# Kernel optimization log

Hardware: AMD Instinct MI355X
Metric: run time of the kernel (lower is better)

## Reference

```python
import jax, jax.numpy as jnp
import numpy as np

N, E, R, F_IN, F_OUT = 50000, 800000, 6, 128, 128


def setup_inputs() -> dict:
    key = jax.random.key(0)
    ks = jax.random.split(key, 9)
    return {
        "node_h": jax.random.normal(ks[0], (N, F_IN), jnp.float32),
        "weight": jax.random.normal(ks[1], (R, F_IN, F_OUT), jnp.float32) * 0.05,
        "att1": jax.random.normal(ks[2], (F_OUT, 1), jnp.float32),
        "att2": jax.random.normal(ks[3], (F_OUT, 1), jnp.float32),
        "Wc": jax.random.normal(ks[4], (F_OUT, 2 * F_OUT), jnp.float32) * 0.05,
        "bc": jnp.zeros((F_OUT,), jnp.float32),
        "edge_src": jax.random.randint(ks[5], (E,), 0, N, dtype=jnp.int64) if jax.config.jax_enable_x64 else jax.random.randint(ks[5], (E,), 0, N),
        "edge_dst": jax.random.randint(ks[6], (E,), 0, N),
        "edge_rel": jax.random.randint(ks[7], (E,), 0, R),
    }


def reference(node_h, weight, att1, att2, Wc, bc, edge_src, edge_dst, edge_rel):
    n = node_h.shape[0]
    # combined (relation, dst) segment id -> replaces dense per-relation adjacency
    seg = edge_rel * n + edge_dst
    # per-relation incoming degree of each dst node: [R, N]
    deg = jax.ops.segment_sum(
        jnp.ones(edge_src.shape, jnp.float32), seg, num_segments=R * n
    ).reshape(R, n)
    # per-relation transformed features hrd[r] = h @ W[r]: [R, N, O]
    hrd = jnp.einsum('nf,rfo->rno', node_h, weight)
    # per-edge message = hrd[rel_e, src_e]: [E, O]
    msg = hrd[edge_rel, edge_src]
    # scatter-sum into (rel, dst) then normalize by 1/(1 + deg_r(dst))
    agg = jax.ops.segment_sum(msg, seg, num_segments=R * n).reshape(R, n, F_OUT)
    hrs = agg / (1.0 + deg)[:, :, None]
    op = jnp.transpose(hrs, (1, 0, 2))  # [N, R, O]
    # two attention heads: softmax over the relation axis
    s1 = jax.nn.softmax(op @ att1, axis=1)  # [N, R, 1]
    s2 = jax.nn.softmax(op @ att2, axis=1)
    h_comb = jnp.concatenate([op * s1, op * s2], axis=-1)  # [N, R, 2O]
    h5 = h_comb @ Wc.T + bc  # attention_concat linear: [N, R, O]
    h = jnp.sum(h5, axis=1)  # sum over relations: [N, O]
    return (h, weight)
```

## Files before the change

### kernel.cpp

```cpp
#include <hip/hip_runtime.h>

#define NN 50000
#define NE 800000
#define NR 6
#define FD 128
#define NS (NN * NR)
#define MB ((NS + 1023) / 1024)

typedef __attribute__((ext_vector_type(8))) short bf16x8;
typedef __attribute__((ext_vector_type(4))) float f32x4;

__device__ __forceinline__ unsigned short f2bf(float x) {
    unsigned u = __float_as_uint(x);
    u += 0x7FFFu + ((u >> 16) & 1u);
    return (unsigned short)(u >> 16);
}
__device__ __forceinline__ unsigned pack2bf(float lo, float hi) {
    return (unsigned)f2bf(lo) | ((unsigned)f2bf(hi) << 16);
}
__device__ __forceinline__ float bf_lo(unsigned u) { return __uint_as_float(u << 16); }
__device__ __forceinline__ float bf_hi(unsigned u) { return __uint_as_float(u & 0xFFFF0000u); }

__global__ __launch_bounds__(256) void k_cast(
    const float* __restrict__ node_h, unsigned* __restrict__ nh2)
{
    int i = (blockIdx.x * 256 + threadIdx.x) * 8;
    float4 a = *(const float4*)(node_h + i);
    float4 b = *(const float4*)(node_h + i + 4);
    uint4 o;
    o.x = pack2bf(a.x, a.y); o.y = pack2bf(a.z, a.w);
    o.z = pack2bf(b.x, b.y); o.w = pack2bf(b.z, b.w);
    *(uint4*)(nh2 + i / 2) = o;
}

__global__ __launch_bounds__(256) void k_hist(
    const int* __restrict__ edst, const int* __restrict__ erel,
    int* __restrict__ cnt)
{
    int e = blockIdx.x * 256 + threadIdx.x;
    if (e < NE) atomicAdd(cnt + edst[e] * NR + erel[e], 1);
}

__global__ __launch_bounds__(256) void k_bsum(
    const int* __restrict__ cnt, int* __restrict__ bsum)
{
    __shared__ int red[256];
    const int b = blockIdx.x, t = threadIdx.x;
    int idx0 = b * 1024 + t * 4;
    int4 c = *(const int4*)(cnt + idx0);
    int s = 0;
    if (idx0 + 0 < NS) s += c.x;
    if (idx0 + 1 < NS) s += c.y;
    if (idx0 + 2 < NS) s += c.z;
    if (idx0 + 3 < NS) s += c.w;
    red[t] = s;
    __syncthreads();
    for (int off = 128; off > 0; off >>= 1) {
        if (t < off) red[t] += red[t + off];
        __syncthreads();
    }
    if (t == 0) bsum[b] = red[0];
}

__global__ __launch_bounds__(512) void k_scanb(
    const int* __restrict__ bsum, int* __restrict__ bpre)
{
    __shared__ int s[512];
    const int t = threadIdx.x;
    int v = (t < MB) ? bsum[t] : 0;
    s[t] = v;
    __syncthreads();
    for (int off = 1; off < 512; off <<= 1) {
        int x = (t >= off) ? s[t - off] : 0;
        __syncthreads();
        if (t >= off) s[t] += x;
        __syncthreads();
    }
    bpre[t] = s[t] - v;
}

__global__ __launch_bounds__(256) void k_scan3(
    const int* __restrict__ cnt, const int* __restrict__ bpre,
    int* __restrict__ offs, int* __restrict__ cursor)
{
    __shared__ int partial[256];
    const int b = blockIdx.x, t = threadIdx.x;
    int idx0 = b * 1024 + t * 4;
    int4 c = *(const int4*)(cnt + idx0);
    if (idx0 + 0 >= NS) c.x = 0;
    if (idx0 + 1 >= NS) c.y = 0;
    if (idx0 + 2 >= NS) c.z = 0;
    if (idx0 + 3 >= NS) c.w = 0;
    int tsum = c.x + c.y + c.z + c.w;
    partial[t] = tsum;
    __syncthreads();
    for (int off = 1; off < 256; off <<= 1) {
        int x = (t >= off) ? partial[t - off] : 0;
        __syncthreads();
        if (t >= off) partial[t] += x;
        __syncthreads();
    }
    int base = bpre[b] + partial[t] - tsum;
    int4 o;
    o.x = base;
    o.y = base + c.x;
    o.z = base + c.x + c.y;
    o.w = base + c.x + c.y + c.z;
    if (idx0 + 3 < NS) {
        *(int4*)(offs + idx0) = o;
        *(int4*)(cursor + idx0) = o;
    } else {
        int v[4] = {o.x, o.y, o.z, o.w};
        for (int k = 0; k < 4; ++k)
            if (idx0 + k < NS) { offs[idx0 + k] = v[k]; cursor[idx0 + k] = v[k]; }
    }
    if (b == 0 && t == 0) offs[NS] = NE;
}

__global__ __launch_bounds__(256) void k_place(
    const int* __restrict__ esrc, const int* __restrict__ edst,
    const int* __restrict__ erel, int* __restrict__ cursor,
    int* __restrict__ eidx)
{
    int e = blockIdx.x * 256 + threadIdx.x;
    if (e >= NE) return;
    int seg = edst[e] * NR + erel[e];
    int pos = atomicAdd(cursor + seg, 1);
    eidx[pos] = esrc[e];
}

__global__ __launch_bounds__(256) void k_prep_w(
    const float* __restrict__ weight,
    const float* __restrict__ att1, const float* __restrict__ att2,
    float* __restrict__ w1, float* __restrict__ w2)
{
    __shared__ float a1s[FD], a2s[FD];
    const int r = blockIdx.x;
    const int t = threadIdx.x;
    if (t < FD) { a1s[t] = att1[t]; a2s[t] = att2[t]; }
    __syncthreads();
    int f = t & 127;
    const float* av = (t < FD) ? a1s : a2s;
    float* wo = (t < FD) ? w1 : w2;
    const float* Wrow = weight + ((size_t)r * FD + f) * FD;
    float acc = 0.f;
#pragma unroll 8
    for (int o = 0; o < FD; ++o) acc += Wrow[o] * av[o];
    wo[r * FD + f] = acc;
}

__global__ __launch_bounds__(256) void k_prep_U(
    const float* __restrict__ weight, const float* __restrict__ Wc,
    short* __restrict__ Upk)
{
    __shared__ float As[64 * 65];
    __shared__ float Bs[64 * 132];
    const int h  = blockIdx.y / NR;
    const int r  = blockIdx.y % NR;
    const int f0 = blockIdx.x * 64;
    const int t  = threadIdx.x;
    const int tm = t & 15, tn = t >> 4;

    float acc[4][8];
#pragma unroll
    for (int i = 0; i < 4; ++i)
#pragma unroll
        for (int j = 0; j < 8; ++j) acc[i][j] = 0.f;

    for (int kt = 0; kt < 2; ++kt) {
#pragma unroll
        for (int i = 0; i < 4; ++i) {
            int flat = i * 1024 + t * 4;
            int row = flat >> 6, k = flat & 63;
            float4 v = *(const float4*)(weight + ((size_t)r * FD + f0 + row) * FD + kt * 64 + k);
            float* p = As + row * 65 + k;
            p[0] = v.x; p[1] = v.y; p[2] = v.z; p[3] = v.w;
        }
#pragma unroll
        for (int i = 0; i < 8; ++i) {
            int flat4 = i * 256 + t;
            int o = flat4 >> 4, j4 = flat4 & 15;
            float4 v = *(const float4*)(Wc + (size_t)o * 256 + h * FD + kt * 64 + j4 * 4);
            float* p = Bs + (j4 * 4) * 132 + o;
            p[0] = v.x; p[132] = v.y; p[264] = v.z; p[396] = v.w;
        }
        __syncthreads();
#pragma unroll 4
        for (int k = 0; k < 64; ++k) {
            float aa[4];
#pragma unroll
            for (int i = 0; i < 4; ++i) aa[i] = As[(4 * tm + i) * 65 + k];
            float4 blo = *(const float4*)(Bs + k * 132 + 8 * tn);
            float4 bhi = *(const float4*)(Bs + k * 132 + 8 * tn + 4);
            float bb[8] = {blo.x, blo.y, blo.z, blo.w, bhi.x, bhi.y, bhi.z, bhi.w};
#pragma unroll
            for (int i = 0; i < 4; ++i)
#pragma unroll
                for (int j = 0; j < 8; ++j) acc[i][j] += aa[i] * bb[j];
        }
        __syncthreads();
    }

#pragma unroll
    for (int i = 0; i < 4; ++i)
#pragma unroll
        for (int j = 0; j < 8; ++j) {
            int f = f0 + 4 * tm + i, o = 8 * tn + j;
            int kstep = f >> 5, g = (f >> 3) & 3, jj = f & 7;
            int nt = o >> 4, ln = g * 16 + (o & 15);
            size_t sidx = ((((size_t)(h * NR + r) * 4 + kstep) * 8 + nt) * 64 + ln) * 8 + jj;
            Upk[sidx] = (short)f2bf(acc[i][j]);
        }
}

__global__ __launch_bounds__(256) void k_agg(
    const unsigned* __restrict__ nh2,
    const int* __restrict__ offs,
    const int* __restrict__ eidx,
    const float* __restrict__ w1v, const float* __restrict__ w2v,
    unsigned* __restrict__ aggp,
    float* __restrict__ s1o, float* __restrict__ s2o)
{
    const int t = threadIdx.x;
    const int lane = t & 63;
    const int grp = lane >> 4;
    const int fl  = lane & 15;
    const int d = blockIdx.x * 4 + (t >> 6);
    if (d >= NN) return;

    float p1v[2], p2v[2];

#pragma unroll
    for (int pass = 0; pass < 2; ++pass) {
        const int r = pass * 4 + grp;
        float q1 = 0.f, q2 = 0.f;
        if (r < NR) {
            const int sbeg = offs[d * NR + r];
            const int send = offs[d * NR + r + 1];
            float a0 = 0.f, a1 = 0.f, a2 = 0.f, a3 = 0.f;
            float a4 = 0.f, a5 = 0.f, a6 = 0.f, a7 = 0.f;
            for (int j = sbeg; j < send; ++j) {
                int s = eidx[j];
                uint4 v = *(const uint4*)(nh2 + (size_t)s * 64 + fl * 4);
                a0 += bf_lo(v.x); a1 += bf_hi(v.x);
                a2 += bf_lo(v.y); a3 += bf_hi(v.y);
                a4 += bf_lo(v.z); a5 += bf_hi(v.z);
                a6 += bf_lo(v.w); a7 += bf_hi(v.w);
            }
            float sc = 1.0f / (1.0f + (float)(send - sbeg));
            a0 *= sc; a1 *= sc; a2 *= sc; a3 *= sc;
            a4 *= sc; a5 *= sc; a6 *= sc; a7 *= sc;
            uint4 o;
            o.x = pack2bf(a0, a1); o.y = pack2bf(a2, a3);
            o.z = pack2bf(a4, a5); o.w = pack2bf(a6, a7);
            *(uint4*)(aggp + ((size_t)r * NN + d) * 64 + fl * 4) = o;
            float4 wa = *(const float4*)(w1v + r * FD + fl * 8);
            float4 wb = *(const float4*)(w1v + r * FD + fl * 8 + 4);
            float4 wc = *(const float4*)(w2v + r * FD + fl * 8);
            float4 wd = *(const float4*)(w2v + r * FD + fl * 8 + 4);
            q1 = a0 * wa.x + a1 * wa.y + a2 * wa.z + a3 * wa.w
               + a4 * wb.x + a5 * wb.y + a6 * wb.z + a7 * wb.w;
            q2 = a0 * wc.x + a1 * wc.y + a2 * wc.z + a3 * wc.w
               + a4 * wd.x + a5 * wd.y + a6 * wd.z + a7 * wd.w;
        }
#pragma unroll
        for (int off = 1; off < 16; off <<= 1) {
            q1 += __shfl_xor(q1, off, 64);
            q2 += __shfl_xor(q2, off, 64);
        }
        p1v[pass] = q1; p2v[pass] = q2;
    }

    float p1[NR], p2[NR];
#pragma unroll
    for (int r = 0; r < 4; ++r) {
        p1[r] = __shfl(p1v[0], r * 16, 64);
        p2[r] = __shfl(p2v[0], r * 16, 64);
    }
    p1[4] = __shfl(p1v[1], 0, 64);  p1[5] = __shfl(p1v[1], 16, 64);
    p2[4] = __shfl(p2v[1], 0, 64);  p2[5] = __shfl(p2v[1], 16, 64);

    float m1 = p1[0], m2 = p2[0];
#pragma unroll
    for (int r = 1; r < NR; ++r) { m1 = fmaxf(m1, p1[r]); m2 = fmaxf(m2, p2[r]); }
    float e1[NR], e2[NR], d1 = 0.f, d2 = 0.f;
#pragma unroll
    for (int r = 0; r < NR; ++r) {
        e1[r] = __expf(p1[r] - m1); d1 += e1[r];
        e2[r] = __expf(p2[r] - m2); d2 += e2[r];
    }
    d1 = 1.0f / d1; d2 = 1.0f / d2;
    if (lane == 0) {
#pragma unroll
        for (int r = 0; r < NR; ++r) {
            s1o[d * NR + r] = e1[r] * d1;
            s2o[d * NR + r] = e2[r] * d2;
        }
    }
}

__global__ __launch_bounds__(256, 4) void k_fused(
    const unsigned* __restrict__ aggp,
    const float* __restrict__ s1, const float* __restrict__ s2,
    const short* __restrict__ Upk,
    const float* __restrict__ bc,
    float* __restrict__ out)
{
    __shared__ short Al[64 * 128];
    __shared__ float sl[2 * 64 * NR];
    const int n0 = blockIdx.x * 64;
    const int t = threadIdx.x;
    const int lane = t & 63;
    const int w = t >> 6;

    for (int i = t; i < 2 * 64 * NR; i += 256) {
        int h = i / (64 * NR);
        int rr = i % (64 * NR);
        int row = rr / NR, r = rr % NR;
        int n = n0 + row;
        float v = 0.f;
        if (n < NN) v = (h ? s2 : s1)[(size_t)n * NR + r];
        sl[i] = v;
    }

    f32x4 acc[8];
#pragma unroll
    for (int nt = 0; nt < 8; ++nt) acc[nt] = (f32x4){0.f, 0.f, 0.f, 0.f};

    const int m = w * 16 + (lane & 15);
    const int g = lane >> 4;

    for (int r = 0; r < NR; ++r) {
        __syncthreads();
        {
            int row = t >> 2, kq = t & 3;
            int n = n0 + row;
            const unsigned* src = aggp + ((size_t)r * NN + n) * 64 + kq * 16;
#pragma unroll
            for (int c = 0; c < 4; ++c) {
                uint4 v = make_uint4(0, 0, 0, 0);
                if (n < NN) v = *(const uint4*)(src + c * 4);
                int ks = kq * 32 + c * 8;
                int addr = row * 128 + (ks ^ ((row & 7) << 3));
                *(uint4*)&Al[addr] = v;
            }
        }
        __syncthreads();

#pragma unroll
        for (int h = 0; h < 2; ++h) {
            f32x4 ar[8];
#pragma unroll
            for (int nt = 0; nt < 8; ++nt) ar[nt] = (f32x4){0.f, 0.f, 0.f, 0.f};
#pragma unroll
            for (int kstep = 0; kstep < 4; ++kstep) {
                bf16x8 af = *(const bf16x8*)&Al[m * 128 + ((kstep * 32 + g * 8) ^ ((m & 7) << 3))];
                const short* Ub = Upk + (((size_t)(h * NR + r) * 4 + kstep) * 8) * 64 * 8 + lane * 8;
#pragma unroll
                for (int nt = 0; nt < 8; ++nt) {
                    bf16x8 bfr = *(const bf16x8*)(Ub + nt * 64 * 8);
                    ar[nt] = __builtin_amdgcn_mfma_f32_16x16x32_bf16(af, bfr, ar[nt], 0, 0, 0);
                }
            }
            float sv[4];
#pragma unroll
            for (int reg = 0; reg < 4; ++reg)
                sv[reg] = sl[h * 64 * NR + (w * 16 + (lane >> 4) * 4 + reg) * NR + r];
#pragma unroll
            for (int nt = 0; nt < 8; ++nt)
#pragma unroll
                for (int reg = 0; reg < 4; ++reg)
                    acc[nt][reg] += sv[reg] * ar[nt][reg];
        }
    }

    const int rowbase = n0 + w * 16 + (lane >> 4) * 4;
    const int col0 = lane & 15;
#pragma unroll
    for (int nt = 0; nt < 8; ++nt) {
        int col = nt * 16 + col0;
        float b6 = 6.0f * bc[col];
#pragma unroll
        for (int reg = 0; reg < 4; ++reg) {
            int n = rowbase + reg;
            if (n < NN) out[(size_t)n * FD + col] = acc[nt][reg] + b6;
        }
    }
}

extern "C" void kernel_launch(void* const* d_in, const int* in_sizes, int n_in,
                              void* d_out, int out_size, void* d_ws, size_t ws_size,
                              hipStream_t stream)
{
    const float* node_h = (const float*)d_in[0];
    const float* weight = (const float*)d_in[1];
    const float* att1   = (const float*)d_in[2];
    const float* att2   = (const float*)d_in[3];
    const float* Wc     = (const float*)d_in[4];
    const float* bc     = (const float*)d_in[5];
    const int* esrc = (const int*)d_in[6];
    const int* edst = (const int*)d_in[7];
    const int* erel = (const int*)d_in[8];
    float* out = (float*)d_out;

    char* wsp = (char*)d_ws;
    auto alloc = [&](size_t bytes) {
        char* p = wsp;
        wsp += (bytes + 255) & ~(size_t)255;
        return p;
    };
    unsigned* aggp = (unsigned*)alloc((size_t)NR * NN * 64 * 4);
    unsigned* nh2  = (unsigned*)alloc((size_t)NN * 64 * 4);
    short* Upk     = (short*)alloc((size_t)2 * NR * FD * FD * 2);
    float* w1      = (float*)alloc(NR * FD * 4);
    float* w2      = (float*)alloc(NR * FD * 4);
    float* s1      = (float*)alloc((size_t)NN * NR * 4);
    float* s2      = (float*)alloc((size_t)NN * NR * 4);
    int* offs      = (int*)alloc((size_t)(NS + 1 + 64) * 4);
    int* cursor    = (int*)alloc((size_t)(NS + 2048) * 4);
    int* bsum      = (int*)alloc(512 * 4);
    int* bpre      = (int*)alloc(512 * 4);
    int* eidx      = (int*)d_out;

    hipMemsetAsync(cursor, 0, (size_t)NS * sizeof(int), stream);

    k_hist<<<(NE + 255) / 256, 256, 0, stream>>>(edst, erel, cursor);
    k_bsum<<<MB, 256, 0, stream>>>(cursor, bsum);
    k_scanb<<<1, 512, 0, stream>>>(bsum, bpre);
    k_scan3<<<MB, 256, 0, stream>>>(cursor, bpre, offs, cursor);
    k_place<<<(NE + 255) / 256, 256, 0, stream>>>(esrc, edst, erel, cursor, eidx);

    k_cast<<<(NN * FD / 8 + 255) / 256, 256, 0, stream>>>(node_h, nh2);
    k_prep_w<<<NR, 256, 0, stream>>>(weight, att1, att2, w1, w2);
    k_prep_U<<<dim3(2, 2 * NR), 256, 0, stream>>>(weight, Wc, Upk);

    k_agg<<<(NN + 3) / 4, 256, 0, stream>>>(nh2, offs, eidx, w1, w2, aggp, s1, s2);

    k_fused<<<(NN + 63) / 64, 256, 0, stream>>>(aggp, s1, s2, Upk, bc, out);

    hipMemcpyAsync(out + (size_t)NN * FD, weight,
                   (size_t)NR * FD * FD * sizeof(float),
                   hipMemcpyDeviceToDevice, stream);
}
```

Before: 355.1 us.

## Split fused epilogue over output column halves and load A fragments directly

The fused projection kernel now launches a second grid dimension, so each block computes 64 of the 128 output columns, halving per-thread accumulators and doubling block count. The LDS staging of the aggregated rows, with its per-relation barriers, is replaced by each lane loading its bf16 A fragments straight from global memory. Both column-half blocks read the same A rows, so global/L2 traffic for the aggregate doubles. In exchange the kernel gets lower register pressure, more parallelism and no per-relation syncs.

New measurement: 348.8 us. Within noise of the previous version (-1.8%).

```diff
diff --git a/kernel.cpp b/kernel.cpp
--- a/kernel.cpp
+++ b/kernel.cpp
@@ -299,16 +299,16 @@
     }
 }
 
-__global__ __launch_bounds__(256, 4) void k_fused(
+__global__ __launch_bounds__(256) void k_fused(
     const unsigned* __restrict__ aggp,
     const float* __restrict__ s1, const float* __restrict__ s2,
     const short* __restrict__ Upk,
     const float* __restrict__ bc,
     float* __restrict__ out)
 {
-    __shared__ short Al[64 * 128];
     __shared__ float sl[2 * 64 * NR];
     const int n0 = blockIdx.x * 64;
+    const int ch = blockIdx.y;
     const int t = threadIdx.x;
     const int lane = t & 63;
     const int w = t >> 6;
@@ -322,63 +322,55 @@
         if (n < NN) v = (h ? s2 : s1)[(size_t)n * NR + r];
         sl[i] = v;
     }
-
-    f32x4 acc[8];
-#pragma unroll
-    for (int nt = 0; nt < 8; ++nt) acc[nt] = (f32x4){0.f, 0.f, 0.f, 0.f};
-
-    const int m = w * 16 + (lane & 15);
+    __syncthreads();
+
+    const int mrow = min(n0 + w * 16 + (lane & 15), NN - 1);
     const int g = lane >> 4;
+    const unsigned* arow = aggp + (size_t)mrow * 64 + g * 4;
+
+    f32x4 acc[4];
+#pragma unroll
+    for (int nt = 0; nt < 4; ++nt) acc[nt] = (f32x4){0.f, 0.f, 0.f, 0.f};
+
+    const int rl4 = w * 16 + (lane >> 4) * 4;
 
     for (int r = 0; r < NR; ++r) {
-        __syncthreads();
-        {
-            int row = t >> 2, kq = t & 3;
-            int n = n0 + row;
-            const unsigned* src = aggp + ((size_t)r * NN + n) * 64 + kq * 16;
-#pragma unroll
-            for (int c = 0; c < 4; ++c) {
-                uint4 v = make_uint4(0, 0, 0, 0);
-                if (n < NN) v = *(const uint4*)(src + c * 4);
-                int ks = kq * 32 + c * 8;
-                int addr = row * 128 + (ks ^ ((row & 7) << 3));
-                *(uint4*)&Al[addr] = v;
-            }
-        }
-        __syncthreads();
+        bf16x8 af[4];
+#pragma unroll
+        for (int kstep = 0; kstep < 4; ++kstep)
+            af[kstep] = *(const bf16x8*)(arow + (size_t)r * (NN * 64) + kstep * 16);
 
 #pragma unroll
         for (int h = 0; h < 2; ++h) {
-            f32x4 ar[8];
-#pragma unroll
-            for (int nt = 0; nt < 8; ++nt) ar[nt] = (f32x4){0.f, 0.f, 0.f, 0.f};
+            f32x4 ar[4];
+#pragma unroll
+            for (int nt = 0; nt < 4; ++nt) ar[nt] = (f32x4){0.f, 0.f, 0.f, 0.f};
+            const short* Ub = Upk + ((size_t)(h * NR + r) * 4) * 8 * 512 + lane * 8;
 #pragma unroll
             for (int kstep = 0; kstep < 4; ++kstep) {
-                bf16x8 af = *(const bf16x8*)&Al[m * 128 + ((kstep * 32 + g * 8) ^ ((m & 7) << 3))];
-                const short* Ub = Upk + (((size_t)(h * NR + r) * 4 + kstep) * 8) * 64 * 8 + lane * 8;
-#pragma unroll
-                for (int nt = 0; nt < 8; ++nt) {
-                    bf16x8 bfr = *(const bf16x8*)(Ub + nt * 64 * 8);
-                    ar[nt] = __builtin_amdgcn_mfma_f32_16x16x32_bf16(af, bfr, ar[nt], 0, 0, 0);
+#pragma unroll
+                for (int nt = 0; nt < 4; ++nt) {
+                    bf16x8 bfr = *(const bf16x8*)(Ub + ((size_t)kstep * 8 + ch * 4 + nt) * 512);
+                    ar[nt] = __builtin_amdgcn_mfma_f32_16x16x32_bf16(af[kstep], bfr, ar[nt], 0, 0, 0);
                 }
             }
             float sv[4];
 #pragma unroll
             for (int reg = 0; reg < 4; ++reg)
-                sv[reg] = sl[h * 64 * NR + (w * 16 + (lane >> 4) * 4 + reg) * NR + r];
-#pragma unroll
-            for (int nt = 0; nt < 8; ++nt)
+                sv[reg] = sl[h * 64 * NR + (rl4 + reg) * NR + r];
+#pragma unroll
+            for (int nt = 0; nt < 4; ++nt)
 #pragma unroll
                 for (int reg = 0; reg < 4; ++reg)
                     acc[nt][reg] += sv[reg] * ar[nt][reg];
         }
     }
 
-    const int rowbase = n0 + w * 16 + (lane >> 4) * 4;
-    const int col0 = lane & 15;
-#pragma unroll
-    for (int nt = 0; nt < 8; ++nt) {
-        int col = nt * 16 + col0;
+    const int rowbase = n0 + rl4;
+    const int col0 = ch * 64 + (lane & 15);
+#pragma unroll
+    for (int nt = 0; nt < 4; ++nt) {
+        int col = col0 + nt * 16;
         float b6 = 6.0f * bc[col];
 #pragma unroll
         for (int reg = 0; reg < 4; ++reg) {
@@ -436,7 +428,8 @@
 
     k_agg<<<(NN + 3) / 4, 256, 0, stream>>>(nh2, offs, eidx, w1, w2, aggp, s1, s2);
 
-    k_fused<<<(NN + 63) / 64, 256, 0, stream>>>(aggp, s1, s2, Upk, bc, out);
+    dim3 gf((NN + 63) / 64, 2);
+    k_fused<<<gf, 256, 0, stream>>>(aggp, s1, s2, Upk, bc, out);
 
     hipMemcpyAsync(out + (size_t)NN * FD, weight,
                    (size_t)NR * FD * FD * sizeof(float),
```
